# Optimization experiments

Hardware: AMD Instinct MI355X
Metric: run time of the kernel (lower is better)

Reference implementation:

```python
import jax, jax.numpy as jnp
import numpy as np

N_NODES = 50000
N_EDGES = 800000
HID = 128
DEPTH = 10
N_GRAPHS = 512
IN_F = 32


def setup_inputs() -> dict:
    key = jax.random.key(0)
    ks = jax.random.split(key, 12)
    x = jax.random.normal(ks[0], (N_NODES, IN_F), jnp.float32)
    edge_index = jax.random.randint(ks[1], (2, N_EDGES), 0, N_NODES, dtype=jnp.int32)
    batch_map = jnp.sort(jax.random.randint(ks[2], (N_NODES,), 0, N_GRAPHS, dtype=jnp.int32))
    # parameters (PyG GraphConv: lin_rel has bias, lin_root has no bias)
    W_embed = jax.random.normal(ks[3], (IN_F, HID), jnp.float32) * 0.1
    W_rel = jax.random.normal(ks[4], (DEPTH, HID, HID), jnp.float32) * 0.05
    b_rel = jax.random.normal(ks[5], (DEPTH, HID), jnp.float32) * 0.01
    W_root = jax.random.normal(ks[6], (DEPTH, HID, HID), jnp.float32) * 0.05
    W_ws = jax.random.normal(ks[7], (DEPTH * HID, 1), jnp.float32) * 0.05
    b_ws = jax.random.normal(ks[8], (1,), jnp.float32) * 0.01
    W_sg = jax.random.normal(ks[9], (DEPTH * HID, IN_F), jnp.float32) * 0.05
    b_sg = jax.random.normal(ks[10], (IN_F,), jnp.float32) * 0.01
    return {
        "x": x, "edge_index": edge_index, "batch_map": batch_map,
        "num_graphs": N_GRAPHS,
        "W_embed": W_embed, "W_rel": W_rel, "b_rel": b_rel, "W_root": W_root,
        "W_ws": W_ws, "b_ws": b_ws, "W_sg": W_sg, "b_sg": b_sg,
    }


def reference(x, edge_index, batch_map, num_graphs,
              W_embed, W_rel, b_rel, W_root, W_ws, b_ws, W_sg, b_sg):
    n = x.shape[0]
    src, dst = edge_index[0], edge_index[1]
    h = x @ W_embed  # [N, 128]
    reps = []
    for i in range(DEPTH):
        # PyG GraphConv (aggr='add'): lin_rel(sum_j h_j) + lin_root(h_i)
        agg = jax.ops.segment_sum(h[src], dst, num_segments=n)  # [N, 128]
        h = agg @ W_rel[i] + b_rel[i] + h @ W_root[i]
        reps.append(h)
    out = jnp.concatenate(reps, axis=1)  # [N, 1280]
    # softmax over last dim of [N,1] logits (faithful: yields ones)
    sum_w = jax.nn.softmax(out @ W_ws + b_ws, axis=-1)  # [N, 1]
    out = sum_w * out
    pooled = jax.ops.segment_sum(out, batch_map, num_segments=num_graphs)  # [G, 1280]
    return pooled @ W_sg + b_sg  # [G, 32]
```

## Files before the change

kernel.cpp:

```cpp
#include <hip/hip_runtime.h>

#define N_NODES 50000
#define N_EDGES 800000
#define HID 128
#define DEPTH 10
#define N_GRAPHS 512
#define IN_F 32

#define BM 128
#define GBLK (50048 / BM)
#define PADN 50048

#define ROWW 256

#define SB 256
#define NSB ((N_NODES + SB - 1) / SB)

#define NBIN 8
#define BINW ((N_NODES + NBIN - 1) / NBIN)
#define NCH 500
#define CHSZ (N_EDGES / NCH)

#define NBT 20
#define NAST 12
#define PACK_CHUNKS (DEPTH * NBT * 512)

typedef __attribute__((ext_vector_type(8))) short short8;
typedef __attribute__((ext_vector_type(4))) float f32x4;
typedef __attribute__((ext_vector_type(4))) unsigned uint4v;

__device__ __forceinline__ float bf2f(short u) {
    union { unsigned i; float f; } v; v.i = ((unsigned)(unsigned short)u) << 16; return v.f;
}
__device__ __forceinline__ short f2bf(float f) {
    union { float f; unsigned i; } v; v.f = f;
    unsigned r = (v.i + 0x7FFFu + ((v.i >> 16) & 1u)) >> 16;
    return (short)r;
}
__device__ __forceinline__ unsigned pack2(short lo, short hi) {
    return ((unsigned)(unsigned short)hi << 16) | (unsigned)(unsigned short)lo;
}

__global__ __launch_bounds__(256) void pack_weights(
    const float* __restrict__ Wrel, const float* __restrict__ Wroot,
    short* __restrict__ Bp) {
    int idx = blockIdx.x * 256 + threadIdx.x;
    if (idx >= PACK_CHUNKS) return;
    int layer = idx / (NBT * 512);
    int rem = idx - layer * NBT * 512;
    int t = rem >> 9;
    int c = rem & 511;
    int kslot = c >> 7, n = c & 127;
    int kc, lo;
    const float* W;
    if (t < 8)       { kc = t >> 1;        W = Wrel;  lo = t & 1; }
    else if (t < 12) { kc = t - 8;         W = Wrel;  lo = 0; }
    else             { kc = (t - 12) >> 1; W = Wroot; lo = t & 1; }
    W += (size_t)layer * HID * HID;
    short out[8];
#pragma unroll
    for (int j = 0; j < 8; ++j) {
        int k = kc * 32 + kslot * 8 + j;
        float v = W[(size_t)k * HID + n];
        short hi = f2bf(v);
        if (lo) { v = v - bf2f(hi); hi = f2bf(v); }
        out[j] = hi;
    }
    *reinterpret_cast<short8*>(Bp + (size_t)idx * 8) = *reinterpret_cast<short8*>(out);
}

__global__ __launch_bounds__(128) void embed_kernel(
    const float* __restrict__ x, const float* __restrict__ W,
    short* __restrict__ hIL) {
    __shared__ float Ws[IN_F * HID];
    int t = threadIdx.x;
    for (int i = t; i < IN_F * HID; i += 128) Ws[i] = W[i];
    __syncthreads();
    int nbeg = blockIdx.x * 50;
    for (int n = nbeg; n < nbeg + 50; ++n) {
        float acc = 0.f;
#pragma unroll
        for (int k = 0; k < IN_F; ++k)
            acc += x[(size_t)n * IN_F + k] * Ws[k * HID + t];
        short hh = f2bf(acc);
        hIL[(size_t)n * ROWW + t] = hh;
        hIL[(size_t)n * ROWW + HID + t] = f2bf(acc - bf2f(hh));
    }
}

__global__ __launch_bounds__(256) void hist8_kernel(
    const int* __restrict__ dst, int* __restrict__ counts8) {
    int e = blockIdx.x * 256 + threadIdx.x;
    int plane = blockIdx.x & 7;
    if (e < N_EDGES) atomicAdd(&counts8[(size_t)plane * N_NODES + dst[e]], 1);
}

__global__ __launch_bounds__(SB) void scan_part1(
    const int* __restrict__ counts8, int* __restrict__ counts,
    int* __restrict__ bsum, int n) {
    __shared__ int s[SB];
    int t = threadIdx.x;
    int i = blockIdx.x * SB + t;
    int v = 0;
    if (i < n) {
#pragma unroll
        for (int p = 0; p < 8; ++p) v += counts8[(size_t)p * N_NODES + i];
        counts[i] = v;
    }
    s[t] = v;
    __syncthreads();
    for (int off = SB / 2; off >= 1; off >>= 1) {
        if (t < off) s[t] += s[t + off];
        __syncthreads();
    }
    if (t == 0) bsum[blockIdx.x] = s[0];
}

__global__ __launch_bounds__(256) void scan_part2(
    const int* __restrict__ bsum, int* __restrict__ boff, int nb) {
    __shared__ int s[256];
    int t = threadIdx.x;
    int v0 = (t < nb) ? bsum[t] : 0;
    s[t] = v0;
    __syncthreads();
    for (int off = 1; off < 256; off <<= 1) {
        int v = (t >= off) ? s[t - off] : 0;
        __syncthreads();
        s[t] += v;
        __syncthreads();
    }
    boff[t] = (t == 0) ? 0 : s[t - 1];
}

__global__ __launch_bounds__(SB) void scan_part3(
    const int* __restrict__ count, const int* __restrict__ boff,
    int* __restrict__ ptr, int* __restrict__ cursor, int n) {
    __shared__ int s[SB];
    int b = blockIdx.x, t = threadIdx.x;
    int i = b * SB + t;
    int v = (i < n) ? count[i] : 0;
    s[t] = v;
    __syncthreads();
    for (int off = 1; off < SB; off <<= 1) {
        int u = (t >= off) ? s[t - off] : 0;
        __syncthreads();
        s[t] += u;
        __syncthreads();
    }
    int excl = s[t] - v + boff[b];
    if (i < n) {
        ptr[i] = excl;
        cursor[i] = excl;
        if (i == n - 1) ptr[n] = excl + v;
    }
}

__global__ __launch_bounds__(256) void scatter8_kernel(
    const int* __restrict__ src, const int* __restrict__ dst,
    int* __restrict__ cursor, int* __restrict__ sorted_src) {
    int s = blockIdx.x & 7;
    int c = blockIdx.x >> 3;
    int lo = s * BINW;
    int hi = lo + BINW;
    int base = c * CHSZ;
    for (int e = base + threadIdx.x; e < base + CHSZ; e += 256) {
        int d = dst[e];
        int sv = src[e];
        if (d >= lo && d < hi) {
            int p = atomicAdd(&cursor[d], 1);
            sorted_src[p] = sv;
        }
    }
}

__global__ __launch_bounds__(256) void aggregate_kernel(
    const short* __restrict__ hIL, const int* __restrict__ row_ptr,
    const int* __restrict__ sorted_src, short* __restrict__ agg2) {
    int n = (blockIdx.x * 256 + threadIdx.x) >> 6;
    int lane = threadIdx.x & 63;
    const unsigned* __restrict__ R = (const unsigned*)hIL;
    int beg = row_ptr[n], end = row_ptr[n + 1];
    float a0 = 0.f, a1 = 0.f;
#define ACC(v) do { \
        union { unsigned u; float f; } u0, u1; \
        u0.u = (v) << 16; u1.u = (v) & 0xFFFF0000u; \
        a0 += u0.f; a1 += u1.f; } while (0)
    int j = beg;
    for (; j + 8 <= end; j += 8) {
        unsigned v[8];
#pragma unroll
        for (int u = 0; u < 8; ++u) {
            int s = __builtin_amdgcn_readfirstlane(sorted_src[j + u]);
            v[u] = R[(size_t)s * 128 + lane];
        }
#pragma unroll
        for (int u = 0; u < 8; ++u) ACC(v[u]);
    }
    for (; j + 2 <= end; j += 2) {
        int s0 = __builtin_amdgcn_readfirstlane(sorted_src[j]);
        int s1 = __builtin_amdgcn_readfirstlane(sorted_src[j + 1]);
        unsigned v0 = R[(size_t)s0 * 128 + lane];
        unsigned v1 = R[(size_t)s1 * 128 + lane];
        ACC(v0); ACC(v1);
    }
    if (j < end) {
        int s = __builtin_amdgcn_readfirstlane(sorted_src[j]);
        unsigned v = R[(size_t)s * 128 + lane];
        ACC(v);
    }
#undef ACC
    short h0 = f2bf(a0), h1 = f2bf(a1);
    unsigned hw = pack2(h0, h1);
    unsigned lw = pack2(f2bf(a0 - bf2f(h0)), f2bf(a1 - bf2f(h1)));
    ((unsigned*)agg2)[(size_t)n * 128 + lane] = hw;
    ((unsigned*)agg2)[(size_t)n * 128 + 64 + lane] = lw;
}

__global__ __launch_bounds__(512) void layer_gemm_mfma(
    const short* __restrict__ agg2, const short* __restrict__ hIL,
    const short* __restrict__ Bp, const float* __restrict__ bias,
    short* __restrict__ outIL,
    const int* __restrict__ bmap, float* __restrict__ pooled, int layer,
    int write_h) {
    __shared__ __align__(16) char smem[49664];
    short* AbBuf = (short*)smem;
    short* BbBuf = (short*)(smem + 16384);
    float* Cs    = (float*)smem;
    int*   bmapS = (int*)(smem + 49152);

    int tid = threadIdx.x;
    int lane = tid & 63;
    int w = tid >> 6;
    int wr = w >> 2, wc = w & 3;
    int m0 = blockIdx.x * BM;

    int r0 = tid >> 2, q0 = tid & 3;

    f32x4 acc[4][2];
#pragma unroll
    for (int m = 0; m < 4; ++m)
#pragma unroll
        for (int n = 0; n < 2; ++n) acc[m][n] = (f32x4)0.f;

#define NB_OF(a)   (((a) >> 2) == 1 ? 1 : 2)
#define BOFF_OF(a) (((a) < 4) ? (a) * 2 : ((a) < 8) ? 8 + ((a) - 4) : 12 + ((a) - 8) * 2)
#define A_PTR(a)   ((((a) >> 2) <= 1 ? agg2 : hIL) + ((((a) >> 2) == 1) ? HID : 0))

    {
        const short* Ap = A_PTR(0);
        short8 a0 = *reinterpret_cast<const short8*>(Ap + (size_t)(m0 + r0) * ROWW + q0 * 8);
        short8 b0 = *reinterpret_cast<const short8*>(Bp + (size_t)tid * 8);
        short8 b1 = *reinterpret_cast<const short8*>(Bp + (size_t)4096 + (size_t)tid * 8);
        *reinterpret_cast<short8*>(&AbBuf[(q0 * 128 + r0) * 8]) = a0;
        *reinterpret_cast<short8*>(&BbBuf[tid * 8]) = b0;
        *reinterpret_cast<short8*>(&BbBuf[4096 + tid * 8]) = b1;
    }
    __syncthreads();

    int kb = lane >> 4;
    int rr = lane & 15;

    for (int a = 0; a < NAST; ++a) {
        int cur = a & 1;
        int nb = NB_OF(a);
        short8 an, bn0, bn1;
        int nbn = 0;
        if (a < NAST - 1) {
            int na = a + 1;
            nbn = NB_OF(na);
            int kc = (na & 3) * 32;
            const short* Ap = A_PTR(na) + kc;
            an = *reinterpret_cast<const short8*>(Ap + (size_t)(m0 + r0) * ROWW + q0 * 8);
            const short* Bsrc = Bp + (size_t)BOFF_OF(na) * 4096;
            bn0 = *reinterpret_cast<const short8*>(Bsrc + (size_t)tid * 8);
            if (nbn == 2)
                bn1 = *reinterpret_cast<const short8*>(Bsrc + (size_t)4096 + (size_t)tid * 8);
        }
        short8 af[4];
#pragma unroll
        for (int m = 0; m < 4; ++m)
            af[m] = *reinterpret_cast<const short8*>(&AbBuf[cur * 4096 + (kb * 128 + wr * 64 + m * 16 + rr) * 8]);
#pragma unroll
        for (int j = 0; j < 2; ++j) {
            if (j < nb) {
                short8 bfr[2];
#pragma unroll
                for (int n = 0; n < 2; ++n)
                    bfr[n] = *reinterpret_cast<const short8*>(
                        &BbBuf[cur * 8192 + j * 4096 + (kb * 128 + wc * 32 + n * 16 + rr) * 8]);
#pragma unroll
                for (int m = 0; m < 4; ++m)
#pragma unroll
                    for (int n = 0; n < 2; ++n)
                        acc[m][n] = __builtin_amdgcn_mfma_f32_16x16x32_bf16(af[m], bfr[n], acc[m][n], 0, 0, 0);
            }
        }
        if (a < NAST - 1) {
            int nxt = cur ^ 1;
            *reinterpret_cast<short8*>(&AbBuf[nxt * 4096 + (q0 * 128 + r0) * 8]) = an;
            *reinterpret_cast<short8*>(&BbBuf[nxt * 8192 + tid * 8]) = bn0;
            if (nbn == 2)
                *reinterpret_cast<short8*>(&BbBuf[nxt * 8192 + 4096 + tid * 8]) = bn1;
        }
        __syncthreads();
    }
#undef NB_OF
#undef BOFF_OF
#undef A_PTR

    if (tid < 128) {
        int gi = m0 + tid;
        bmapS[tid] = bmap[gi < N_NODES ? gi : N_NODES - 1];
    }
    float bs[2];
    {
        int col = wc * 32 + rr;
#pragma unroll
        for (int n = 0; n < 2; ++n) bs[n] = bias[col + n * 16];
    }
    int colP = tid & 127;
    int quarter = tid >> 7;

    for (int c = 0; c < 2; ++c) {
        if (wr == c) {
            int colb = wc * 32 + rr;
#pragma unroll
            for (int m = 0; m < 4; ++m) {
#pragma unroll
                for (int n = 0; n < 2; ++n) {
#pragma unroll
                    for (int i = 0; i < 4; ++i) {
                        int lr = m * 16 + kb * 4 + i;
                        Cs[lr * 132 + colb + n * 16] = acc[m][n][i] + bs[n];
                    }
                }
            }
        }
        __syncthreads();

        if (write_h) {
#pragma unroll
            for (int pq = 0; pq < 2; ++pq) {
                int idx = pq * 512 + tid;
                int lr = idx >> 4;
                int oct = idx & 15;
                const float4* crow = reinterpret_cast<const float4*>(&Cs[lr * 132 + oct * 8]);
                float4 c0 = crow[0], c1 = crow[1];
                float v[8] = {c0.x, c0.y, c0.z, c0.w, c1.x, c1.y, c1.z, c1.w};
                unsigned hw[4], lw[4];
#pragma unroll
                for (int k = 0; k < 4; ++k) {
                    short ha = f2bf(v[2 * k]), hb = f2bf(v[2 * k + 1]);
                    short la = f2bf(v[2 * k] - bf2f(ha)), lb = f2bf(v[2 * k + 1] - bf2f(hb));
                    hw[k] = pack2(ha, hb);
                    lw[k] = pack2(la, lb);
                }
                int row = m0 + c * 64 + lr;
                unsigned* oI = (unsigned*)(outIL + (size_t)row * ROWW);
                uint4v hv; hv.x = hw[0]; hv.y = hw[1]; hv.z = hw[2]; hv.w = hw[3];
                uint4v lv; lv.x = lw[0]; lv.y = lw[1]; lv.z = lw[2]; lv.w = lw[3];
                *reinterpret_cast<uint4v*>(oI + oct * 4) = hv;
                *reinterpret_cast<uint4v*>(oI + 64 + oct * 4) = lv;
            }
        }

        {
            float pacc = 0.f;
            int gprev = -1;
            float* pbase = pooled + (size_t)layer * HID + colP;
            for (int q = 0; q < 16; ++q) {
                int lr = quarter * 16 + q;
                int grow = m0 + c * 64 + lr;
                if (grow >= N_NODES) break;
                int g = bmapS[c * 64 + lr];
                float v = Cs[lr * 132 + colP];
                if (g != gprev) {
                    if (gprev >= 0) atomicAdd(pbase + (size_t)gprev * (DEPTH * HID), pacc);
                    gprev = g; pacc = v;
                } else {
                    pacc += v;
                }
            }
            if (gprev >= 0) atomicAdd(pbase + (size_t)gprev * (DEPTH * HID), pacc);
        }
        __syncthreads();
    }
}

__global__ __launch_bounds__(256) void final_kernel(
    const float* __restrict__ pooled, const float* __restrict__ Wsg,
    const float* __restrict__ bsg, float* __restrict__ out) {
    int t = threadIdx.x & 31;
    int g = blockIdx.x * 8 + (threadIdx.x >> 5);
    float acc = bsg[t];
    const float* prow = pooled + (size_t)g * (DEPTH * HID);
    for (int k = 0; k < DEPTH * HID; ++k)
        acc += prow[k] * Wsg[k * IN_F + t];
    out[g * IN_F + t] = acc;
}

extern "C" void kernel_launch(void* const* d_in, const int* in_sizes, int n_in,
                              void* d_out, int out_size, void* d_ws, size_t ws_size,
                              hipStream_t stream) {
    const float* x       = (const float*)d_in[0];
    const int*   edge    = (const int*)d_in[1];
    const int*   bmap    = (const int*)d_in[2];
    const float* W_embed = (const float*)d_in[4];
    const float* W_rel   = (const float*)d_in[5];
    const float* b_rel   = (const float*)d_in[6];
    const float* W_root  = (const float*)d_in[7];
    const float* W_sg    = (const float*)d_in[10];
    const float* b_sg    = (const float*)d_in[11];
    float* out = (float*)d_out;

    const int* src = edge;
    const int* dst = edge + N_EDGES;

    char* ws = (char*)d_ws;
    auto alloc = [&](size_t bytes) -> char* {
        char* p = ws;
        ws += (bytes + 255) & ~(size_t)255;
        return p;
    };
    const size_t rowB = (size_t)PADN * ROWW * 2;
    short* h_a    = (short*)alloc(rowB);
    short* h_b    = (short*)alloc(rowB);
    short* agg2   = (short*)alloc(rowB);
    float* pooled = (float*)alloc((size_t)N_GRAPHS * DEPTH * HID * 4);
    int* counts8    = (int*)alloc((size_t)8 * N_NODES * 4);
    int* counts     = (int*)alloc((size_t)N_NODES * 4);
    int* row_ptr    = (int*)alloc((size_t)(N_NODES + 1) * 4);
    int* cursor     = (int*)alloc((size_t)N_NODES * 4);
    int* sorted_src = (int*)alloc((size_t)N_EDGES * 4);
    int* bsum       = (int*)alloc((size_t)256 * 4);
    int* boff       = (int*)alloc((size_t)256 * 4);
    short* Bpacked  = (short*)alloc((size_t)PACK_CHUNKS * 8 * 2);

    hipMemsetAsync(counts8, 0, (size_t)8 * N_NODES * 4, stream);
    hipMemsetAsync(pooled, 0, (size_t)N_GRAPHS * DEPTH * HID * 4, stream);

    pack_weights<<<(PACK_CHUNKS + 255) / 256, 256, 0, stream>>>(W_rel, W_root, Bpacked);
    embed_kernel<<<1000, 128, 0, stream>>>(x, W_embed, h_a);

    hist8_kernel<<<(N_EDGES + 255) / 256, 256, 0, stream>>>(dst, counts8);
    scan_part1<<<NSB, SB, 0, stream>>>(counts8, counts, bsum, N_NODES);
    scan_part2<<<1, 256, 0, stream>>>(bsum, boff, NSB);
    scan_part3<<<NSB, SB, 0, stream>>>(counts, boff, row_ptr, cursor, N_NODES);
    scatter8_kernel<<<NBIN * NCH, 256, 0, stream>>>(src, dst, cursor, sorted_src);

    short *hc = h_a, *hn = h_b;
    for (int i = 0; i < DEPTH; ++i) {
        aggregate_kernel<<<(N_NODES + 3) / 4, 256, 0, stream>>>(hc, row_ptr, sorted_src, agg2);
        layer_gemm_mfma<<<GBLK, 512, 0, stream>>>(agg2, hc,
                                                  Bpacked + (size_t)i * NBT * 4096,
                                                  b_rel + (size_t)i * HID,
                                                  hn, bmap, pooled, i,
                                                  (i < DEPTH - 1) ? 1 : 0);
        short* t = hc; hc = hn; hn = t;
    }

    final_kernel<<<N_GRAPHS / 8, 256, 0, stream>>>(pooled, W_sg, b_sg, out);
}
```

Baseline: 681.2 us.

## Gather neighbor features from column-sliced bf16 copy with lane-group edge splitting

```diff
diff --git a/kernel.cpp b/kernel.cpp
--- a/kernel.cpp
+++ b/kernel.cpp
@@ -71,7 +71,7 @@
 
 __global__ __launch_bounds__(128) void embed_kernel(
     const float* __restrict__ x, const float* __restrict__ W,
-    short* __restrict__ hIL) {
+    short* __restrict__ hIL, short* __restrict__ hSl) {
     __shared__ float Ws[IN_F * HID];
     int t = threadIdx.x;
     for (int i = t; i < IN_F * HID; i += 128) Ws[i] = W[i];
@@ -85,6 +85,7 @@
         short hh = f2bf(acc);
         hIL[(size_t)n * ROWW + t] = hh;
         hIL[(size_t)n * ROWW + HID + t] = f2bf(acc - bf2f(hh));
+        hSl[((size_t)(t >> 5) * PADN + n) * 32 + (t & 31)] = hh;
     }
 }
 
@@ -173,53 +174,58 @@
     }
 }
 
-__global__ __launch_bounds__(256) void aggregate_kernel(
-    const short* __restrict__ hIL, const int* __restrict__ row_ptr,
+__global__ __launch_bounds__(512) void aggregate_sliced(
+    const short* __restrict__ hSl, const int* __restrict__ row_ptr,
     const int* __restrict__ sorted_src, short* __restrict__ agg2) {
-    int n = (blockIdx.x * 256 + threadIdx.x) >> 6;
+    int bid = blockIdx.x;
+    int s2 = (bid & 7) >> 1;
+    int chunk = bid >> 3;
+    int wid = threadIdx.x >> 6;
     int lane = threadIdx.x & 63;
-    const unsigned* __restrict__ R = (const unsigned*)hIL;
+    int n = chunk * 8 + wid;
+    if (n >= N_NODES) return;
+    int g = lane >> 4;
+    int u = lane & 15;
+    const unsigned* __restrict__ R = (const unsigned*)hSl + (size_t)s2 * PADN * 16;
     int beg = row_ptr[n], end = row_ptr[n + 1];
     float a0 = 0.f, a1 = 0.f;
 #define ACC(v) do { \
-        union { unsigned u; float f; } u0, u1; \
-        u0.u = (v) << 16; u1.u = (v) & 0xFFFF0000u; \
-        a0 += u0.f; a1 += u1.f; } while (0)
-    int j = beg;
-    for (; j + 8 <= end; j += 8) {
-        unsigned v[8];
-#pragma unroll
-        for (int u = 0; u < 8; ++u) {
-            int s = __builtin_amdgcn_readfirstlane(sorted_src[j + u]);
-            v[u] = R[(size_t)s * 128 + lane];
-        }
-#pragma unroll
-        for (int u = 0; u < 8; ++u) ACC(v[u]);
-    }
-    for (; j + 2 <= end; j += 2) {
-        int s0 = __builtin_amdgcn_readfirstlane(sorted_src[j]);
-        int s1 = __builtin_amdgcn_readfirstlane(sorted_src[j + 1]);
-        unsigned v0 = R[(size_t)s0 * 128 + lane];
-        unsigned v1 = R[(size_t)s1 * 128 + lane];
-        ACC(v0); ACC(v1);
-    }
-    if (j < end) {
-        int s = __builtin_amdgcn_readfirstlane(sorted_src[j]);
-        unsigned v = R[(size_t)s * 128 + lane];
-        ACC(v);
+        union { unsigned uu; float ff; } q0, q1; \
+        q0.uu = (v) << 16; q1.uu = (v) & 0xFFFF0000u; \
+        a0 += q0.ff; a1 += q1.ff; } while (0)
+    int j = beg + g;
+    for (; j + 12 < end; j += 16) {
+        int i0 = sorted_src[j];
+        int i1 = sorted_src[j + 4];
+        int i2 = sorted_src[j + 8];
+        int i3 = sorted_src[j + 12];
+        unsigned v0 = R[(size_t)i0 * 16 + u];
+        unsigned v1 = R[(size_t)i1 * 16 + u];
+        unsigned v2 = R[(size_t)i2 * 16 + u];
+        unsigned v3 = R[(size_t)i3 * 16 + u];
+        ACC(v0); ACC(v1); ACC(v2); ACC(v3);
+    }
+    for (; j < end; j += 4) {
+        int i0 = sorted_src[j];
+        unsigned v0 = R[(size_t)i0 * 16 + u];
+        ACC(v0);
     }
 #undef ACC
+    a0 += __shfl_xor(a0, 16); a1 += __shfl_xor(a1, 16);
+    a0 += __shfl_xor(a0, 32); a1 += __shfl_xor(a1, 32);
     short h0 = f2bf(a0), h1 = f2bf(a1);
-    unsigned hw = pack2(h0, h1);
-    unsigned lw = pack2(f2bf(a0 - bf2f(h0)), f2bf(a1 - bf2f(h1)));
-    ((unsigned*)agg2)[(size_t)n * 128 + lane] = hw;
-    ((unsigned*)agg2)[(size_t)n * 128 + 64 + lane] = lw;
+    if (lane < 16) {
+        ((unsigned*)agg2)[(size_t)n * 128 + s2 * 16 + u] = pack2(h0, h1);
+    } else if (lane < 32) {
+        unsigned lw = pack2(f2bf(a0 - bf2f(h0)), f2bf(a1 - bf2f(h1)));
+        ((unsigned*)agg2)[(size_t)n * 128 + 64 + s2 * 16 + u] = lw;
+    }
 }
 
 __global__ __launch_bounds__(512) void layer_gemm_mfma(
     const short* __restrict__ agg2, const short* __restrict__ hIL,
     const short* __restrict__ Bp, const float* __restrict__ bias,
-    short* __restrict__ outIL,
+    short* __restrict__ outIL, short* __restrict__ outSl,
     const int* __restrict__ bmap, float* __restrict__ pooled, int layer,
     int write_h) {
     __shared__ __align__(16) char smem[49664];
@@ -361,6 +367,9 @@
                 uint4v lv; lv.x = lw[0]; lv.y = lw[1]; lv.z = lw[2]; lv.w = lw[3];
                 *reinterpret_cast<uint4v*>(oI + oct * 4) = hv;
                 *reinterpret_cast<uint4v*>(oI + 64 + oct * 4) = lv;
+                int slice = oct >> 2, sub = oct & 3;
+                unsigned* oS = (unsigned*)outSl + ((size_t)slice * PADN + row) * 16 + sub * 4;
+                *reinterpret_cast<uint4v*>(oS) = hv;
             }
         }
 
@@ -423,8 +432,10 @@
         return p;
     };
     const size_t rowB = (size_t)PADN * ROWW * 2;
+    const size_t slB  = (size_t)4 * PADN * 32 * 2;
     short* h_a    = (short*)alloc(rowB);
     short* h_b    = (short*)alloc(rowB);
+    short* hSl    = (short*)alloc(slB);
     short* agg2   = (short*)alloc(rowB);
     float* pooled = (float*)alloc((size_t)N_GRAPHS * DEPTH * HID * 4);
     int* counts8    = (int*)alloc((size_t)8 * N_NODES * 4);
@@ -440,7 +451,7 @@
     hipMemsetAsync(pooled, 0, (size_t)N_GRAPHS * DEPTH * HID * 4, stream);
 
     pack_weights<<<(PACK_CHUNKS + 255) / 256, 256, 0, stream>>>(W_rel, W_root, Bpacked);
-    embed_kernel<<<1000, 128, 0, stream>>>(x, W_embed, h_a);
+    embed_kernel<<<1000, 128, 0, stream>>>(x, W_embed, h_a, hSl);
 
     hist8_kernel<<<(N_EDGES + 255) / 256, 256, 0, stream>>>(dst, counts8);
     scan_part1<<<NSB, SB, 0, stream>>>(counts8, counts, bsum, N_NODES);
@@ -450,11 +461,11 @@
 
     short *hc = h_a, *hn = h_b;
     for (int i = 0; i < DEPTH; ++i) {
-        aggregate_kernel<<<(N_NODES + 3) / 4, 256, 0, stream>>>(hc, row_ptr, sorted_src, agg2);
+        aggregate_sliced<<<((N_NODES + 7) / 8) * 8, 512, 0, stream>>>(hSl, row_ptr, sorted_src, agg2);
         layer_gemm_mfma<<<GBLK, 512, 0, stream>>>(agg2, hc,
                                                   Bpacked + (size_t)i * NBT * 4096,
                                                   b_rel + (size_t)i * HID,
-                                                  hn, bmap, pooled, i,
+                                                  hn, hSl, bmap, pooled, i,
                                                   (i < DEPTH - 1) ? 1 : 0);
         short* t = hc; hc = hn; hn = t;
     }
```

Result: slower. 1.738 ms (+155.2%).
